# Kernel optimization log

Hardware: AMD Instinct MI355X
Metric: run time of the kernel (lower is better)

The kernel has to match this reference:

```python
import jax, jax.numpy as jnp
import numpy as np

DIM = 512
HEADS = 8
DIM_HEAD = 64
HIDDEN = HEADS * DIM_HEAD  # 512
B, C, H, W = 32, DIM, 32, 32


def setup_inputs() -> dict:
    key = jax.random.key(0)
    ks = jax.random.split(key, 7)
    s_in = 1.0 / np.sqrt(DIM)
    s_h = 1.0 / np.sqrt(HIDDEN)
    x = jax.random.normal(ks[0], (B, C, H, W), dtype=jnp.float32)
    Wq = jax.random.uniform(ks[1], (DIM, HIDDEN), jnp.float32, -s_in, s_in)
    Wk = jax.random.uniform(ks[2], (DIM, HIDDEN), jnp.float32, -s_in, s_in)
    Wv = jax.random.uniform(ks[3], (DIM, HIDDEN), jnp.float32, -s_in, s_in)
    Wp = jax.random.uniform(ks[4], (HIDDEN, DIM), jnp.float32, -s_h, s_h)
    bp = jax.random.uniform(ks[5], (DIM,), jnp.float32, -s_h, s_h)
    return {"x": x, "Wq": Wq, "Wk": Wk, "Wv": Wv, "Wp": Wp, "bp": bp}


def reference(x, Wq, Wk, Wv, Wp, bp):
    b, c, h, w = x.shape
    n = h * w
    xt = x.reshape(b, c, n).transpose(0, 2, 1)  # [B, N, C]
    q = (xt @ Wq).reshape(b, n, HEADS, DIM_HEAD)
    k = (xt @ Wk).reshape(b, n, HEADS, DIM_HEAD)
    v = (xt @ Wv).reshape(b, n, HEADS, DIM_HEAD)
    k_softmax = jax.nn.softmax(k, axis=1)  # softmax over tokens N
    context = jnp.einsum('bnhd,bnhv->bhdv', k_softmax, v)  # [B, H, D, D]
    out = jnp.einsum('bnhd,bhdv->bnhv', q, context).reshape(b, n, HIDDEN)
    out = out @ Wp + bp  # [B, N, C]
    return out.transpose(0, 2, 1).reshape(b, c, h, w)
```

## Files before the change

### kernel.cpp

```cpp
#include <hip/hip_runtime.h>
#include <hip/hip_bf16.h>


__device__ __forceinline__ float bf2f(unsigned short u) {
    union { unsigned int i; float f; } x;
    x.i = ((unsigned int)u) << 16;
    return x.f;
}
__device__ __forceinline__ unsigned short f2bf(float f) {
    unsigned int u = __float_as_uint(f);
    unsigned int lsb = (u >> 16) & 1u;
    u += 0x7fffu + lsb;
    return (unsigned short)(u >> 16);
}
__device__ __forceinline__ float waveReduceMax(float v) {
    #pragma unroll
    for (int off = 32; off > 0; off >>= 1) v = fmaxf(v, __shfl_xor(v, off, 64));
    return v;
}
__device__ __forceinline__ float waveReduceSum(float v) {
    #pragma unroll
    for (int off = 32; off > 0; off >>= 1) v += __shfl_xor(v, off, 64);
    return v;
}

__device__ __forceinline__ void glds16(const unsigned short* g, unsigned short* l) {
    __builtin_amdgcn_global_load_lds(
        (const __attribute__((address_space(1))) unsigned int*)g,
        (__attribute__((address_space(3))) unsigned int*)l,
        16, 0, 0);
}

typedef __bf16 bf16x8 __attribute__((ext_vector_type(8)));
typedef float  f32x4  __attribute__((ext_vector_type(4)));

__global__ void detect_dtype(const unsigned short* __restrict__ x, int* __restrict__ flag)
{
    int t = threadIdx.x;
    unsigned short u = x[2 * t];
    int e = (u >> 7) & 0xFF;
    int sane = (e >= 113 && e <= 142) ? 1 : 0;
    #pragma unroll
    for (int off = 32; off > 0; off >>= 1) sane += __shfl_xor(sane, off, 64);
    if (t == 0) *flag = (sane >= 32) ? 1 : 0;
}

__global__ __launch_bounds__(256) void transpose_x(
    const void* __restrict__ in, unsigned short* __restrict__ out,
    const int* __restrict__ flag)
{
    const int fl = *flag;
    const int b  = blockIdx.z;
    const int c0 = blockIdx.x * 64;
    const int r0 = blockIdx.y * 64;
    __shared__ unsigned short Ts[64][68];
    const int t   = threadIdx.x;
    const int tr  = t >> 4;
    const int tc4 = (t & 15) * 4;
    #pragma unroll
    for (int rr = 0; rr < 4; ++rr) {
        int rl = rr * 16 + tr;
        long off = (long)b * 524288 + (long)(r0 + rl) * 1024 + c0 + tc4;
        unsigned short v[4];
        if (fl) {
            ushort4 u = *(const ushort4*)((const unsigned short*)in + off);
            v[0] = u.x; v[1] = u.y; v[2] = u.z; v[3] = u.w;
        } else {
            float4 u = *(const float4*)((const float*)in + off);
            v[0] = f2bf(u.x); v[1] = f2bf(u.y); v[2] = f2bf(u.z); v[3] = f2bf(u.w);
        }
        #pragma unroll
        for (int q = 0; q < 4; ++q) Ts[tc4 + q][rl] = v[q];
    }
    __syncthreads();
    #pragma unroll
    for (int rr = 0; rr < 4; ++rr) {
        int cl = rr * 16 + tr;
        ushort4 o = *(const ushort4*)&Ts[cl][tc4];
        *(ushort4*)(out + (long)b * 524288 + (long)(c0 + cl) * 512 + r0 + tc4) = o;
    }
}

__global__ __launch_bounds__(256) void transpose_w3(
    const void* __restrict__ w0, const void* __restrict__ w1,
    const void* __restrict__ w2, unsigned short* __restrict__ out,
    unsigned short* __restrict__ wqb,
    const int* __restrict__ flag)
{
    const int fl = *flag;
    const int z  = blockIdx.z;
    const void* in = (z == 0) ? w0 : (z == 1) ? w1 : w2;
    unsigned short* op = out + (long)z * 262144;
    const int c0 = blockIdx.x * 64;
    const int r0 = blockIdx.y * 64;
    __shared__ unsigned short Ts[64][68];
    const int t   = threadIdx.x;
    const int tr  = t >> 4;
    const int tc4 = (t & 15) * 4;
    #pragma unroll
    for (int rr = 0; rr < 4; ++rr) {
        int rl = rr * 16 + tr;
        long off = (long)(r0 + rl) * 512 + c0 + tc4;
        unsigned short v[4];
        if (fl) {
            ushort4 u = *(const ushort4*)((const unsigned short*)in + off);
            v[0] = u.x; v[1] = u.y; v[2] = u.z; v[3] = u.w;
        } else {
            float4 u = *(const float4*)((const float*)in + off);
            v[0] = f2bf(u.x); v[1] = f2bf(u.y); v[2] = f2bf(u.z); v[3] = f2bf(u.w);
        }
        if (z == 0) {
            ushort4 s; s.x = v[0]; s.y = v[1]; s.z = v[2]; s.w = v[3];
            *(ushort4*)(wqb + off) = s;
        }
        #pragma unroll
        for (int q = 0; q < 4; ++q) Ts[tc4 + q][rl] = v[q];
    }
    __syncthreads();
    #pragma unroll
    for (int rr = 0; rr < 4; ++rr) {
        int cl = rr * 16 + tr;
        ushort4 o = *(const ushort4*)&Ts[cl][tc4];
        *(ushort4*)(op + (long)(c0 + cl) * 512 + r0 + tc4) = o;
    }
}

__global__ __launch_bounds__(256) void gemm_bt_mfma(
    const unsigned short* __restrict__ A, long a_bstride,
    const unsigned short* __restrict__ Bm, long b_bstride,
    void* __restrict__ C, long c_bstride,
    const void* __restrict__ bias,
    int M, int N, int K, int mode,
    const int* __restrict__ flag)
{
    const int b  = blockIdx.z;
    const int n0 = blockIdx.x * 128;
    const int m0 = blockIdx.y * 128;
    const unsigned short* Ab = A  + (long)b * a_bstride;
    const unsigned short* Bb = Bm + (long)b * b_bstride;

    __shared__ unsigned short As[2 * 128 * 32];
    __shared__ unsigned short Bs[2 * 128 * 32];

    const int t    = threadIdx.x;
    const int w    = t >> 6;
    const int lane = t & 63;
    const int wm   = (w & 1) * 64;
    const int wn   = (w >> 1) * 64;
    const int fm   = lane & 15;
    const int kg   = lane >> 4;

    const int crow = lane >> 2;
    const int ccol = (lane & 3) * 8;

    f32x4 acc[4][4] = {};

    #pragma unroll
    for (int j = 0; j < 2; ++j) {
        const int chunk = w * 2 + j;
        const int row   = chunk * 16 + crow;
        glds16(Ab + (long)(m0 + row) * K + ccol, &As[chunk * 512]);
        glds16(Bb + (long)(n0 + row) * K + ccol, &Bs[chunk * 512]);
    }

    int cur = 0;
    for (int k0 = 0; k0 < K; k0 += 32) {
        __syncthreads();

        if (k0 + 32 < K) {
            const int kn  = k0 + 32;
            const int nxt = (cur ^ 1) * 4096;
            #pragma unroll
            for (int j = 0; j < 2; ++j) {
                const int chunk = w * 2 + j;
                const int row   = chunk * 16 + crow;
                glds16(Ab + (long)(m0 + row) * K + kn + ccol, &As[nxt + chunk * 512]);
                glds16(Bb + (long)(n0 + row) * K + kn + ccol, &Bs[nxt + chunk * 512]);
            }
        }

        const int bufo = cur * 4096;
        bf16x8 af[4], bf[4];
        #pragma unroll
        for (int i = 0; i < 4; ++i)
            af[i] = *(const bf16x8*)&As[bufo + (wm + i * 16 + fm) * 32 + kg * 8];
        #pragma unroll
        for (int j = 0; j < 4; ++j)
            bf[j] = *(const bf16x8*)&Bs[bufo + (wn + j * 16 + fm) * 32 + kg * 8];
        #pragma unroll
        for (int i = 0; i < 4; ++i)
            #pragma unroll
            for (int j = 0; j < 4; ++j)
                acc[i][j] = __builtin_amdgcn_mfma_f32_16x16x32_bf16(
                    bf[j], af[i], acc[i][j], 0, 0, 0);
        cur ^= 1;
    }

    const int fl = *flag;
    const long cb = (long)b * c_bstride;
    #pragma unroll
    for (int i = 0; i < 4; ++i) {
        const int m = m0 + wm + i * 16 + fm;
        float bv = 0.f;
        if (mode == 2 && bias)
            bv = fl ? bf2f(((const unsigned short*)bias)[m])
                    : ((const float*)bias)[m];
        #pragma unroll
        for (int j = 0; j < 4; ++j) {
            const int nb = n0 + wn + j * 16 + kg * 4;
            const long off = cb + (long)m * N + nb;
            if (mode == 0) {
                ushort4 o;
                o.x = f2bf(acc[i][j][0]); o.y = f2bf(acc[i][j][1]);
                o.z = f2bf(acc[i][j][2]); o.w = f2bf(acc[i][j][3]);
                *(ushort4*)&((unsigned short*)C)[off] = o;
            } else if (fl) {
                ushort4 o;
                o.x = f2bf(acc[i][j][0] + bv); o.y = f2bf(acc[i][j][1] + bv);
                o.z = f2bf(acc[i][j][2] + bv); o.w = f2bf(acc[i][j][3] + bv);
                *(ushort4*)&((unsigned short*)C)[off] = o;
            } else {
                float4 o;
                o.x = acc[i][j][0] + bv; o.y = acc[i][j][1] + bv;
                o.z = acc[i][j][2] + bv; o.w = acc[i][j][3] + bv;
                *(float4*)&((float*)C)[off] = o;
            }
        }
    }
}

__global__ __launch_bounds__(256) void softmax_rows(unsigned short* __restrict__ KV)
{
    const long row = blockIdx.x;
    unsigned short* p = KV + ((row >> 9) << 20) + ((row & 511) << 10);
    const int t = threadIdx.x;

    ushort4 raw = *(const ushort4*)(p + t * 4);
    float f[4] = {bf2f(raw.x), bf2f(raw.y), bf2f(raw.z), bf2f(raw.w)};

    float m = fmaxf(fmaxf(f[0], f[1]), fmaxf(f[2], f[3]));
    m = waveReduceMax(m);
    __shared__ float redm[4], reds[4];
    if ((t & 63) == 0) redm[t >> 6] = m;
    __syncthreads();
    m = fmaxf(fmaxf(redm[0], redm[1]), fmaxf(redm[2], redm[3]));

    float e[4], s = 0.f;
    #pragma unroll
    for (int i = 0; i < 4; ++i) { e[i] = expf(f[i] - m); s += e[i]; }
    s = waveReduceSum(s);
    if ((t & 63) == 0) reds[t >> 6] = s;
    __syncthreads();
    s = reds[0] + reds[1] + reds[2] + reds[3];
    const float inv = 1.0f / s;

    ushort4 o;
    o.x = f2bf(e[0] * inv); o.y = f2bf(e[1] * inv);
    o.z = f2bf(e[2] * inv); o.w = f2bf(e[3] * inv);
    *(ushort4*)(p + t * 4) = o;
}

__global__ __launch_bounds__(256) void ctx_mfma(
    const unsigned short* __restrict__ KV, float* __restrict__ ctx)
{
    const int bh = blockIdx.x;
    const unsigned short* Kb = KV + ((long)(bh >> 3) << 20) + (long)(bh & 7) * 65536;
    const unsigned short* Vb = Kb + 524288;

    const int t    = threadIdx.x;
    const int w    = t >> 6;
    const int lane = t & 63;
    const int fm   = lane & 15;
    const int kg   = lane >> 4;

    f32x4 acc[4][4] = {};

    #pragma unroll 2
    for (int c = 0; c < 8; ++c) {
        const int k0 = w * 256 + c * 32;
        bf16x8 af[4], bf[4];
        #pragma unroll
        for (int i = 0; i < 4; ++i)
            af[i] = *(const bf16x8*)(Kb + (long)(i * 16 + fm) * 1024 + k0 + kg * 8);
        #pragma unroll
        for (int j = 0; j < 4; ++j)
            bf[j] = *(const bf16x8*)(Vb + (long)(j * 16 + fm) * 1024 + k0 + kg * 8);
        #pragma unroll
        for (int i = 0; i < 4; ++i)
            #pragma unroll
            for (int j = 0; j < 4; ++j)
                acc[i][j] = __builtin_amdgcn_mfma_f32_16x16x32_bf16(
                    af[i], bf[j], acc[i][j], 0, 0, 0);
    }

    __shared__ float red[64][65];
    for (int ph = 0; ph < 4; ++ph) {
        if (w == ph) {
            #pragma unroll
            for (int i = 0; i < 4; ++i)
                #pragma unroll
                for (int j = 0; j < 4; ++j)
                    #pragma unroll
                    for (int r = 0; r < 4; ++r) {
                        const int m = i * 16 + kg * 4 + r;
                        const int n = j * 16 + fm;
                        if (ph == 0) red[m][n]  = acc[i][j][r];
                        else         red[m][n] += acc[i][j][r];
                    }
        }
        __syncthreads();
    }
    float* cp = ctx + (long)bh * 4096;
    for (int i = t; i < 4096; i += 256) cp[i] = red[i >> 6][i & 63];
}

__global__ __launch_bounds__(256) void weff_kernel(
    const float* __restrict__ ctx,
    const void* __restrict__ Wp,
    unsigned short* __restrict__ WeffT,
    const int* __restrict__ flag)
{
    const int fl = *flag;
    const int c0 = blockIdx.x * 64;
    const int h  = blockIdx.y;
    const int b  = blockIdx.z;

    __shared__ float Cs[64][65];
    __shared__ float Ws[64][68];

    const int t = threadIdx.x;
    const int tx = t & 15, ty = t >> 4;

    const float* cb = ctx + ((long)b * 8 + h) * 4096;
    for (int i = t; i < 4096; i += 256) Cs[i >> 6][i & 63] = cb[i];
    for (int i = t; i < 4096; i += 256) {
        int v = i >> 6, c = i & 63;
        long idx = (long)(h * 64 + v) * 512 + c0 + c;
        Ws[v][c] = fl ? bf2f(((const unsigned short*)Wp)[idx])
                      : ((const float*)Wp)[idx];
    }
    __syncthreads();

    float acc[4][4];
    #pragma unroll
    for (int i = 0; i < 4; ++i)
        #pragma unroll
        for (int j = 0; j < 4; ++j) acc[i][j] = 0.f;

    #pragma unroll
    for (int v = 0; v < 64; ++v) {
        float a[4], d[4];
        #pragma unroll
        for (int i = 0; i < 4; ++i) a[i] = Ws[v][ty * 4 + i];
        #pragma unroll
        for (int j = 0; j < 4; ++j) d[j] = Cs[tx * 4 + j][v];
        #pragma unroll
        for (int i = 0; i < 4; ++i)
            #pragma unroll
            for (int j = 0; j < 4; ++j) acc[i][j] += a[i] * d[j];
    }
    #pragma unroll
    for (int i = 0; i < 4; ++i) {
        ushort4 o;
        o.x = f2bf(acc[i][0]); o.y = f2bf(acc[i][1]);
        o.z = f2bf(acc[i][2]); o.w = f2bf(acc[i][3]);
        *(ushort4*)&WeffT[((long)b * 512 + c0 + ty * 4 + i) * 512 + h * 64 + tx * 4] = o;
    }
}

extern "C" void kernel_launch(void* const* d_in, const int* in_sizes, int n_in,
                              void* d_out, int out_size, void* d_ws, size_t ws_size,
                              hipStream_t stream) {
    const void* x  = d_in[0];
    const void* Wq = d_in[1];
    const void* Wk = d_in[2];
    const void* Wv = d_in[3];
    const void* Wp = d_in[4];
    const void* bp = d_in[5];

    char* ws = (char*)d_ws;
    unsigned short* Xt    = (unsigned short*)(ws);
    unsigned short* KV    = (unsigned short*)(ws + 33554432ll);
    unsigned short* Ft    = (unsigned short*)(ws + 33554432ll);
    float*          ctx   = (float*)(ws + 100663296ll);
    unsigned short* WeffT = (unsigned short*)(ws + 104857600ll);
    unsigned short* WT    = (unsigned short*)(ws + 121634816ll);
    unsigned short* Wqb   = (unsigned short*)(ws + 123207680ll);
    int*            flag  = (int*)(ws + 123731968ll);

    detect_dtype<<<dim3(1), dim3(64), 0, stream>>>((const unsigned short*)x, flag);

    transpose_x<<<dim3(16, 8, 32), 256, 0, stream>>>(x, Xt, flag);
    transpose_w3<<<dim3(8, 8, 3), 256, 0, stream>>>(Wq, Wk, Wv, WT, Wqb, flag);

    const long XB = 1024ll * 512;
    gemm_bt_mfma<<<dim3(8, 8, 32), 256, 0, stream>>>(
        WT + 262144, 0, Xt, XB, KV, 1048576ll, nullptr, 1024, 1024, 512, 0, flag);

    softmax_rows<<<dim3(16384), 256, 0, stream>>>(KV);
    ctx_mfma<<<dim3(256), 256, 0, stream>>>(KV, ctx);
    weff_kernel<<<dim3(8, 8, 32), 256, 0, stream>>>(ctx, Wp, WeffT, flag);

    gemm_bt_mfma<<<dim3(4, 4, 32), 256, 0, stream>>>(
        WeffT, 262144ll, Wqb, 0, Ft, 262144ll, nullptr, 512, 512, 512, 0, flag);

    gemm_bt_mfma<<<dim3(8, 4, 32), 256, 0, stream>>>(
        Ft, 262144ll, Xt, XB, d_out, 524288ll, bp, 512, 1024, 512, 2, flag);
}
```

Measured before the change: 319.1 us.

## Fuse token softmax of K into context MFMA kernel

Removes the separate softmax_rows kernel and computes per-row max and sum-of-exp inside the context kernel, then applies exp/normalise on the fly while loading K fragments for MFMA. This avoids a full read-modify-write pass over K in global memory and one kernel launch. In exchange the context kernel reads K three times, recomputes exponentials per element, and only runs 256 blocks, so the reduction prologue may be latency-bound.

```diff
diff --git a/kernel.cpp b/kernel.cpp
--- a/kernel.cpp
+++ b/kernel.cpp
@@ -12,16 +12,6 @@
     unsigned int lsb = (u >> 16) & 1u;
     u += 0x7fffu + lsb;
     return (unsigned short)(u >> 16);
-}
-__device__ __forceinline__ float waveReduceMax(float v) {
-    #pragma unroll
-    for (int off = 32; off > 0; off >>= 1) v = fmaxf(v, __shfl_xor(v, off, 64));
-    return v;
-}
-__device__ __forceinline__ float waveReduceSum(float v) {
-    #pragma unroll
-    for (int off = 32; off > 0; off >>= 1) v += __shfl_xor(v, off, 64);
-    return v;
 }
 
 __device__ __forceinline__ void glds16(const unsigned short* g, unsigned short* l) {
@@ -229,38 +219,7 @@
     }
 }
 
-__global__ __launch_bounds__(256) void softmax_rows(unsigned short* __restrict__ KV)
-{
-    const long row = blockIdx.x;
-    unsigned short* p = KV + ((row >> 9) << 20) + ((row & 511) << 10);
-    const int t = threadIdx.x;
-
-    ushort4 raw = *(const ushort4*)(p + t * 4);
-    float f[4] = {bf2f(raw.x), bf2f(raw.y), bf2f(raw.z), bf2f(raw.w)};
-
-    float m = fmaxf(fmaxf(f[0], f[1]), fmaxf(f[2], f[3]));
-    m = waveReduceMax(m);
-    __shared__ float redm[4], reds[4];
-    if ((t & 63) == 0) redm[t >> 6] = m;
-    __syncthreads();
-    m = fmaxf(fmaxf(redm[0], redm[1]), fmaxf(redm[2], redm[3]));
-
-    float e[4], s = 0.f;
-    #pragma unroll
-    for (int i = 0; i < 4; ++i) { e[i] = expf(f[i] - m); s += e[i]; }
-    s = waveReduceSum(s);
-    if ((t & 63) == 0) reds[t >> 6] = s;
-    __syncthreads();
-    s = reds[0] + reds[1] + reds[2] + reds[3];
-    const float inv = 1.0f / s;
-
-    ushort4 o;
-    o.x = f2bf(e[0] * inv); o.y = f2bf(e[1] * inv);
-    o.z = f2bf(e[2] * inv); o.w = f2bf(e[3] * inv);
-    *(ushort4*)(p + t * 4) = o;
-}
-
-__global__ __launch_bounds__(256) void ctx_mfma(
+__global__ __launch_bounds__(256) void ctx_softmax_mfma(
     const unsigned short* __restrict__ KV, float* __restrict__ ctx)
 {
     const int bh = blockIdx.x;
@@ -273,6 +232,51 @@
     const int fm   = lane & 15;
     const int kg   = lane >> 4;
 
+    __shared__ float sm_m[64];
+    __shared__ float sm_inv[64];
+
+    {
+        const int r = t >> 2;
+        const int q = t & 3;
+        const uint4* row = (const uint4*)(Kb + r * 1024 + q * 256);
+        float mx = -3.402823466e+38f;
+        #pragma unroll 8
+        for (int i = 0; i < 32; ++i) {
+            uint4 u = row[i];
+            #pragma unroll
+            for (int z = 0; z < 4; ++z) {
+                unsigned int uu = ((const unsigned int*)&u)[z];
+                float lo = bf2f((unsigned short)(uu & 0xffffu));
+                float hi = bf2f((unsigned short)(uu >> 16));
+                mx = fmaxf(mx, fmaxf(lo, hi));
+            }
+        }
+        mx = fmaxf(mx, __shfl_xor(mx, 1, 64));
+        mx = fmaxf(mx, __shfl_xor(mx, 2, 64));
+        float s = 0.f;
+        #pragma unroll 8
+        for (int i = 0; i < 32; ++i) {
+            uint4 u = row[i];
+            #pragma unroll
+            for (int z = 0; z < 4; ++z) {
+                unsigned int uu = ((const unsigned int*)&u)[z];
+                s += __expf(bf2f((unsigned short)(uu & 0xffffu)) - mx);
+                s += __expf(bf2f((unsigned short)(uu >> 16)) - mx);
+            }
+        }
+        s += __shfl_xor(s, 1, 64);
+        s += __shfl_xor(s, 2, 64);
+        if (q == 0) { sm_m[r] = mx; sm_inv[r] = 1.0f / s; }
+    }
+    __syncthreads();
+
+    float rm[4], ri[4];
+    #pragma unroll
+    for (int i = 0; i < 4; ++i) {
+        rm[i] = sm_m[i * 16 + fm];
+        ri[i] = sm_inv[i * 16 + fm];
+    }
+
     f32x4 acc[4][4] = {};
 
     #pragma unroll 2
@@ -280,8 +284,19 @@
         const int k0 = w * 256 + c * 32;
         bf16x8 af[4], bf[4];
         #pragma unroll
-        for (int i = 0; i < 4; ++i)
-            af[i] = *(const bf16x8*)(Kb + (long)(i * 16 + fm) * 1024 + k0 + kg * 8);
+        for (int i = 0; i < 4; ++i) {
+            uint4 u = *(const uint4*)(Kb + (long)(i * 16 + fm) * 1024 + k0 + kg * 8);
+            unsigned short o[8];
+            #pragma unroll
+            for (int z = 0; z < 4; ++z) {
+                unsigned int uu = ((const unsigned int*)&u)[z];
+                float lo = __expf(bf2f((unsigned short)(uu & 0xffffu)) - rm[i]) * ri[i];
+                float hi = __expf(bf2f((unsigned short)(uu >> 16))     - rm[i]) * ri[i];
+                o[2 * z]     = f2bf(lo);
+                o[2 * z + 1] = f2bf(hi);
+            }
+            af[i] = *(const bf16x8*)o;
+        }
         #pragma unroll
         for (int j = 0; j < 4; ++j)
             bf[j] = *(const bf16x8*)(Vb + (long)(j * 16 + fm) * 1024 + k0 + kg * 8);
@@ -397,8 +412,8 @@
     gemm_bt_mfma<<<dim3(8, 8, 32), 256, 0, stream>>>(
         WT + 262144, 0, Xt, XB, KV, 1048576ll, nullptr, 1024, 1024, 512, 0, flag);
 
-    softmax_rows<<<dim3(16384), 256, 0, stream>>>(KV);
-    ctx_mfma<<<dim3(256), 256, 0, stream>>>(KV, ctx);
+    ctx_softmax_mfma<<<dim3(256), 256, 0, stream>>>(KV, ctx);
+
     weff_kernel<<<dim3(8, 8, 32), 256, 0, stream>>>(ctx, Wp, WeffT, flag);
 
     gemm_bt_mfma<<<dim3(4, 4, 32), 256, 0, stream>>>(
```

Result: no change. 316.4 us (-0.8%).
